# Optimization experiments

Hardware: AMD Instinct MI355X
Metric: run time of the kernel (lower is better)

The kernel has to match this reference:

```python
import jax, jax.numpy as jnp
import numpy as np

B, S, D, H = 2, 2048, 1024, 16
HD = D // H


def setup_inputs() -> dict:
    key = jax.random.key(0)
    ks = jax.random.split(key, 12)
    s = 0.02
    inp = {
        "query": jax.random.normal(ks[0], (B, S, D), dtype=jnp.float32),
        "Wq": jax.random.normal(ks[1], (D, D), dtype=jnp.float32) * s,
        "bq": jnp.zeros((D,), jnp.float32),
        "Wk": jax.random.normal(ks[2], (D, D), dtype=jnp.float32) * s,
        "bk": jnp.zeros((D,), jnp.float32),
        "Wv": jax.random.normal(ks[3], (D, D), dtype=jnp.float32) * s,
        "bv": jnp.zeros((D,), jnp.float32),
        "Wo": jax.random.normal(ks[4], (D, D), dtype=jnp.float32) * s,
        "bo": jnp.zeros((D,), jnp.float32),
        "Wm1": jax.random.normal(ks[5], (D // 4, D), dtype=jnp.float32) * s,
        "bm1": jnp.zeros((D // 4,), jnp.float32),
        "Wm2": jax.random.normal(ks[6], (D, D // 4), dtype=jnp.float32) * s,
        "bm2": jnp.zeros((D,), jnp.float32),
        "dopamine": jnp.ones((1,), jnp.float32),
        "serotonin": jnp.ones((1,), jnp.float32),
        "norepinephrine": jnp.ones((1,), jnp.float32),
        "acetylcholine": jnp.ones((1,), jnp.float32),
        "attention_scale": jnp.ones((1,), jnp.float32),
        "attention_bias": jnp.zeros((1,), jnp.float32),
    }
    return inp


def reference(query, Wq, bq, Wk, bk, Wv, bv, Wo, bo, Wm1, bm1, Wm2, bm2,
              dopamine, serotonin, norepinephrine, acetylcholine,
              attention_scale, attention_bias):
    b, s, d = query.shape
    scale = HD ** -0.5
    split = lambda t: t.reshape(b, s, H, HD).transpose(0, 2, 1, 3)  # [b,h,s,hd]
    q = split(query @ Wq.T + bq)
    k = split(query @ Wk.T + bk)
    v = split(query @ Wv.T + bv)
    scores = jnp.einsum('bhqd,bhkd->bhqk', q, k) * scale
    w = jax.nn.softmax(scores, axis=-1)  # dropout=0 (eval)
    attn = jnp.einsum('bhqk,bhkd->bhqd', w, v)
    # neuromodulation MLP on flattened query, then combined scalar gate
    mod = jax.nn.relu(query @ Wm1.T + bm1) @ Wm2.T + bm2  # [b,s,d]
    gate = (dopamine + serotonin + norepinephrine + acetylcholine) / 4.0  # [1]
    neuro = split(mod * gate)  # [b,h,s,hd]
    attn = (attn * attention_scale + attention_bias) * (1.0 + neuro)
    out = attn.transpose(0, 2, 1, 3).reshape(b, s, d) @ Wo.T + bo
    return out
```

## Files before the change

### kernel.cpp

```cpp
#include <hip/hip_runtime.h>
#include <stdint.h>
#include <math.h>


typedef __attribute__((ext_vector_type(8))) short short8;
typedef __attribute__((ext_vector_type(4))) float floatx4;

#define MFMA16(a, b, c) __builtin_amdgcn_mfma_f32_16x16x32_bf16(a, b, c, 0, 0, 0)

__device__ __forceinline__ unsigned short f2bf(float f) {
    union { float f; uint32_t u; } v; v.f = f;
    uint32_t r = v.u + 0x7fffu + ((v.u >> 16) & 1u);
    return (unsigned short)(r >> 16);
}
__device__ __forceinline__ float bf2f(unsigned short s) {
    union { uint32_t u; float f; } v; v.u = ((uint32_t)s) << 16;
    return v.f;
}

typedef const __attribute__((address_space(1))) void gvoid_t;
typedef __attribute__((address_space(3))) void lvoid_t;
__device__ __forceinline__ void gld16(const void* g, void* l) {
    __builtin_amdgcn_global_load_lds((gvoid_t*)g, (lvoid_t*)l, 16, 0, 0);
}

template<int BN, bool OUTBF>
__device__ __forceinline__ void gemm_core(const unsigned short* __restrict__ A,
                                          const unsigned short* __restrict__ W,
                                          const float* __restrict__ bias,
                                          void* __restrict__ C,
                                          int N, int K, int bm, int bn, bool relu)
{
    constexpr int MT = (BN == 128) ? 4 : 2;
    constexpr int SU = (BN == 128) ? 4 : 3;
    __shared__ __align__(16) unsigned short As[128][32];
    __shared__ __align__(16) unsigned short Ws[BN][32];

    const int tid  = threadIdx.x;
    const int w    = tid >> 6, lane = tid & 63;
    const int ln   = lane & 15, quad = lane >> 4;
    const int wm   = (BN == 128) ? (w >> 1) * 64 : w * 32;
    const int wn   = (BN == 128) ? (w & 1) * 64 : 0;

    floatx4 acc[MT][4] = {};

    for (int k0 = 0; k0 < K; k0 += 32) {
        __syncthreads();
        #pragma unroll
        for (int i = 0; i < SU; i++) {
            const int t = w * SU + i;
            if (t < 8) {
                const int r0  = t * 16;
                const int row = r0 + (lane >> 2);
                const int c   = (lane & 3) ^ ((row >> 1) & 3);
                gld16(&A[(size_t)(bm + row) * K + k0 + c * 8], &As[r0][0]);
            } else {
                const int r0  = (t - 8) * 16;
                const int row = r0 + (lane >> 2);
                const int c   = (lane & 3) ^ ((row >> 1) & 3);
                gld16(&W[(size_t)(bn + row) * K + k0 + c * 8], &Ws[r0][0]);
            }
        }
        __syncthreads();

        short8 af[MT], bf[4];
        #pragma unroll
        for (int mt = 0; mt < MT; mt++) {
            const int row = wm + mt * 16 + ln;
            af[mt] = *(const short8*)&As[row][(quad ^ ((row >> 1) & 3)) * 8];
        }
        #pragma unroll
        for (int nt = 0; nt < 4; nt++) {
            const int row = wn + nt * 16 + ln;
            bf[nt] = *(const short8*)&Ws[row][(quad ^ ((row >> 1) & 3)) * 8];
        }
        #pragma unroll
        for (int mt = 0; mt < MT; mt++)
            #pragma unroll
            for (int nt = 0; nt < 4; nt++)
                acc[mt][nt] = MFMA16(af[mt], bf[nt], acc[mt][nt]);
    }

    float bv[4];
    #pragma unroll
    for (int nt = 0; nt < 4; nt++) bv[nt] = bias[bn + wn + nt * 16 + ln];

    #pragma unroll
    for (int mt = 0; mt < MT; mt++) {
        #pragma unroll
        for (int nt = 0; nt < 4; nt++) {
            #pragma unroll
            for (int r = 0; r < 4; r++) {
                float v = acc[mt][nt][r] + bv[nt];
                if (relu) v = fmaxf(v, 0.f);
                const size_t row = (size_t)bm + wm + mt * 16 + quad * 4 + r;
                const size_t col = (size_t)bn + wn + nt * 16 + ln;
                if (OUTBF) ((unsigned short*)C)[row * N + col] = f2bf(v);
                else       ((float*)C)[row * N + col] = v;
            }
        }
    }
}

__global__ __launch_bounds__(256) void qkv_mlp1_gemm(
    const unsigned short* __restrict__ A,
    const unsigned short* __restrict__ Wq, const unsigned short* __restrict__ Wk,
    const unsigned short* __restrict__ Wv, const unsigned short* __restrict__ Wm1,
    const float* __restrict__ bq, const float* __restrict__ bk,
    const float* __restrict__ bv, const float* __restrict__ bm1,
    unsigned short* __restrict__ Qo, unsigned short* __restrict__ Ko,
    unsigned short* __restrict__ Vo, unsigned short* __restrict__ Ho)
{
    const int bx = blockIdx.x, bm = blockIdx.y * 128;
    const unsigned short* W; const float* bias; unsigned short* C;
    int N, bn; bool relu = false;
    if (bx < 8)       { W = Wq;  bias = bq;  C = Qo; N = 1024; bn = bx * 128; }
    else if (bx < 16) { W = Wk;  bias = bk;  C = Ko; N = 1024; bn = (bx - 8) * 128; }
    else if (bx < 24) { W = Wv;  bias = bv;  C = Vo; N = 1024; bn = (bx - 16) * 128; }
    else              { W = Wm1; bias = bm1; C = Ho; N = 256;  bn = (bx - 24) * 128; relu = true; }
    gemm_core<128, true>(A, W, bias, C, N, 1024, bm, bn, relu);
}

template<bool OUTBF>
__global__ __launch_bounds__(256) void gemm_bn64(const unsigned short* __restrict__ A,
                                                 const unsigned short* __restrict__ W,
                                                 const float* __restrict__ bias,
                                                 void* __restrict__ C, int N, int K)
{
    gemm_core<64, OUTBF>(A, W, bias, C, N, K, blockIdx.y * 128, blockIdx.x * 64, false);
}

__global__ __launch_bounds__(256) void attn_mfma(const unsigned short* __restrict__ Qg,
                                                 const unsigned short* __restrict__ Kg,
                                                 const unsigned short* __restrict__ Vtg,
                                                 const unsigned short* __restrict__ Modg,
                                                 unsigned short* __restrict__ Yg,
                                                 const float* __restrict__ dop,
                                                 const float* __restrict__ ser,
                                                 const float* __restrict__ nor,
                                                 const float* __restrict__ ach,
                                                 const float* __restrict__ asc,
                                                 const float* __restrict__ abi)
{
    __shared__ __align__(16) unsigned short Ks[128][64];
    __shared__ __align__(16) unsigned short Vs[64][128];
    __shared__ __align__(16) unsigned short Ps[4][16][128];

    const int tid = threadIdx.x;
    const int w   = tid >> 6, lane = tid & 63;
    const int ln  = lane & 15, quad = lane >> 4;
    const int qt  = blockIdx.x, h = blockIdx.y, b = blockIdx.z;

    const size_t qrow = (size_t)b * 2048 + qt * 64 + w * 16 + ln;
    const unsigned short* qp = Qg + qrow * 1024 + h * 64;
    const short8 qf0 = *(const short8*)&qp[quad * 8];
    const short8 qf1 = *(const short8*)&qp[32 + quad * 8];

    const size_t kbase = (size_t)b * 2048 * 1024 + h * 64;
    const size_t vbase = (size_t)(b * 16 + h) * 64 * 2048;

    floatx4 o[4] = {};
    float lsum[4] = {0.f, 0.f, 0.f, 0.f};

    for (int kc = 0; kc < 16; kc++) {
        __syncthreads();
        #pragma unroll
        for (int i = 0; i < 8; i++) {
            const int t = w * 8 + i;
            if (t < 16) {
                const int row = t * 8 + (lane >> 3);
                const int c   = (lane & 7) ^ (row & 7);
                gld16(&Kg[kbase + (size_t)(kc * 128 + row) * 1024 + c * 8], &Ks[t * 8][0]);
            } else {
                const int tv  = t - 16;
                const int row = tv * 4 + (lane >> 4);
                const int c   = (lane & 15) ^ (row & 7);
                gld16(&Vtg[vbase + (size_t)row * 2048 + kc * 128 + c * 8], &Vs[tv * 4][0]);
            }
        }
        __syncthreads();

        floatx4 sc[8];
        #pragma unroll
        for (int nt = 0; nt < 8; nt++) {
            const int row = nt * 16 + ln;
            const short8 kf0 = *(const short8*)&Ks[row][((0 + quad) ^ (ln & 7)) * 8];
            const short8 kf1 = *(const short8*)&Ks[row][((4 + quad) ^ (ln & 7)) * 8];
            floatx4 z = {};
            z = MFMA16(qf0, kf0, z);
            z = MFMA16(qf1, kf1, z);
            sc[nt] = z;
        }

        #pragma unroll
        for (int nt = 0; nt < 8; nt++) {
            #pragma unroll
            for (int r = 0; r < 4; r++) {
                const float p = __expf(sc[nt][r] * 0.125f);
                lsum[r] += p;
                const int prow = quad * 4 + r;
                const int col  = nt * 16 + ln;
                const int slot = (col >> 3) ^ (prow & 7);
                Ps[w][prow][slot * 8 + (ln & 7)] = f2bf(p);
            }
        }

        short8 pf[4];
        #pragma unroll
        for (int ks = 0; ks < 4; ks++)
            pf[ks] = *(const short8*)&Ps[w][ln][((4 * ks + quad) ^ (ln & 7)) * 8];

        #pragma unroll
        for (int ntv = 0; ntv < 4; ntv++) {
            const int row = ntv * 16 + ln;
            #pragma unroll
            for (int ks = 0; ks < 4; ks++) {
                const short8 vf = *(const short8*)&Vs[row][((4 * ks + quad) ^ (ln & 7)) * 8];
                o[ntv] = MFMA16(pf[ks], vf, o[ntv]);
            }
        }
    }

    #pragma unroll
    for (int r = 0; r < 4; r++) {
        float s = lsum[r];
        s += __shfl_xor(s, 1); s += __shfl_xor(s, 2);
        s += __shfl_xor(s, 4); s += __shfl_xor(s, 8);
        lsum[r] = 1.f / s;
    }

    const float gate = 0.25f * (dop[0] + ser[0] + nor[0] + ach[0]);
    const float scb = asc[0], bib = abi[0];
    const size_t orow0 = (size_t)b * 2048 + qt * 64 + w * 16;
    #pragma unroll
    for (int ntv = 0; ntv < 4; ntv++) {
        #pragma unroll
        for (int r = 0; r < 4; r++) {
            const size_t row = orow0 + quad * 4 + r;
            const size_t col = (size_t)h * 64 + ntv * 16 + ln;
            const float x  = o[ntv][r] * lsum[r];
            const float mo = bf2f(Modg[row * 1024 + col]);
            const float y  = (x * scb + bib) * (1.f + mo * gate);
            Yg[row * 1024 + col] = f2bf(y);
        }
    }
}

typedef __attribute__((ext_vector_type(8))) unsigned short ushort8;
__global__ __launch_bounds__(256) void transpose_v(const unsigned short* __restrict__ Vb,
                                                   unsigned short* __restrict__ Vt)
{
    __shared__ __align__(16) unsigned short T[64][72];
    const int tid = threadIdx.x;
    const int s0 = blockIdx.x * 64, h = blockIdx.y, b = blockIdx.z;
    const int g = tid & 7;
    #pragma unroll
    for (int p = 0; p < 2; p++) {
        const int row = p * 32 + (tid >> 3);
        const ushort8 v = *(const ushort8*)&Vb[(size_t)(b * 2048 + s0 + row) * 1024 + h * 64 + g * 8];
        *(ushort8*)&T[row][g * 8] = v;
    }
    __syncthreads();
    #pragma unroll
    for (int p = 0; p < 2; p++) {
        const int hd = p * 32 + (tid >> 3);
        ushort8 ov;
        #pragma unroll
        for (int j = 0; j < 8; j++) ov[j] = T[g * 8 + j][hd];
        *(ushort8*)&Vt[((size_t)(b * 16 + h) * 64 + hd) * 2048 + s0 + g * 8] = ov;
    }
}

__global__ __launch_bounds__(256) void fused_cast(
    const float* __restrict__ q,   const float* __restrict__ wq,
    const float* __restrict__ wk,  const float* __restrict__ wv,
    const float* __restrict__ wo,  const float* __restrict__ wm1,
    const float* __restrict__ wm2,
    unsigned short* __restrict__ dq,  unsigned short* __restrict__ dwq,
    unsigned short* __restrict__ dwk, unsigned short* __restrict__ dwv,
    unsigned short* __restrict__ dwo, unsigned short* __restrict__ dwm1,
    unsigned short* __restrict__ dwm2)
{
    const size_t u = (size_t)blockIdx.x * 256 + threadIdx.x;
    const float* src; unsigned short* dst; size_t off;
    if      (u <  524288) { src = q;   dst = dq;   off = u; }
    else if (u <  655360) { src = wq;  dst = dwq;  off = u - 524288; }
    else if (u <  786432) { src = wk;  dst = dwk;  off = u - 655360; }
    else if (u <  917504) { src = wv;  dst = dwv;  off = u - 786432; }
    else if (u < 1048576) { src = wo;  dst = dwo;  off = u - 917504; }
    else if (u < 1081344) { src = wm1; dst = dwm1; off = u - 1048576; }
    else                  { src = wm2; dst = dwm2; off = u - 1081344; }
    const float4* p = (const float4*)src + off * 2;
    const float4 a = p[0], c = p[1];
    ushort8 o;
    o[0] = f2bf(a.x); o[1] = f2bf(a.y); o[2] = f2bf(a.z); o[3] = f2bf(a.w);
    o[4] = f2bf(c.x); o[5] = f2bf(c.y); o[6] = f2bf(c.z); o[7] = f2bf(c.w);
    *(ushort8*)&dst[off * 8] = o;
}

extern "C" void kernel_launch(void* const* d_in, const int* in_sizes, int n_in,
                              void* d_out, int out_size, void* d_ws, size_t ws_size,
                              hipStream_t stream)
{
    const float* query = (const float*)d_in[0];
    const float* Wq  = (const float*)d_in[1];
    const float* bq  = (const float*)d_in[2];
    const float* Wk  = (const float*)d_in[3];
    const float* bk  = (const float*)d_in[4];
    const float* Wv  = (const float*)d_in[5];
    const float* bv  = (const float*)d_in[6];
    const float* Wo  = (const float*)d_in[7];
    const float* bo  = (const float*)d_in[8];
    const float* Wm1 = (const float*)d_in[9];
    const float* bm1 = (const float*)d_in[10];
    const float* Wm2 = (const float*)d_in[11];
    const float* bm2 = (const float*)d_in[12];
    const float* dop = (const float*)d_in[13];
    const float* ser = (const float*)d_in[14];
    const float* nor = (const float*)d_in[15];
    const float* ach = (const float*)d_in[16];
    const float* asc = (const float*)d_in[17];
    const float* abi = (const float*)d_in[18];

    char* ws = (char*)d_ws;
    const size_t MB = 1024 * 1024;
    unsigned short* Qry  = (unsigned short*)(ws);
    unsigned short* Wqb  = (unsigned short*)(ws + 8 * MB);
    unsigned short* Wkb  = (unsigned short*)(ws + 10 * MB);
    unsigned short* Wvb  = (unsigned short*)(ws + 12 * MB);
    unsigned short* Wob  = (unsigned short*)(ws + 14 * MB);
    unsigned short* Wm1b = (unsigned short*)(ws + 16 * MB);
    unsigned short* Wm2b = (unsigned short*)(ws + 16 * MB + 512 * 1024);
    unsigned short* Qb   = (unsigned short*)(ws + 17 * MB);
    unsigned short* Kb   = (unsigned short*)(ws + 25 * MB);
    unsigned short* Vb   = (unsigned short*)(ws + 33 * MB);
    unsigned short* Vt   = (unsigned short*)(ws + 41 * MB);
    unsigned short* Yb   = (unsigned short*)(ws + 49 * MB);
    unsigned short* Hm   = (unsigned short*)(ws + 57 * MB);
    unsigned short* Modb = Vb;

    fused_cast<<<4352, 256, 0, stream>>>(query, Wq, Wk, Wv, Wo, Wm1, Wm2,
                                         Qry, Wqb, Wkb, Wvb, Wob, Wm1b, Wm2b);

    qkv_mlp1_gemm<<<dim3(26, 32), 256, 0, stream>>>(
        Qry, Wqb, Wkb, Wvb, Wm1b, bq, bk, bv, bm1, Qb, Kb, Vb, Hm);

    transpose_v<<<dim3(32, 16, 2), 256, 0, stream>>>(Vb, Vt);

    gemm_bn64<true><<<dim3(16, 32), 256, 0, stream>>>(Hm, Wm2b, bm2, (void*)Modb, 1024, 256);

    attn_mfma<<<dim3(32, 16, 2), 256, 0, stream>>>(Qb, Kb, Vt, Modb, Yb,
                                                   dop, ser, nor, ach, asc, abi);

    gemm_bn64<false><<<dim3(16, 32), 256, 0, stream>>>(Yb, Wob, bo, d_out, 1024, 1024);
}
```

Measured before the change: 271.7 us.

## Double attention query tile per block and compute transposed scores to halve K/V reloads

The attention kernel now handles 128 query rows per block (32 per wave, two 16-row groups), so each K/V tile staged in LDS is reused by twice as many queries and the grid is halved. Scores are computed as K·Q^T so each lane holds four consecutive keys, which are packed into 8-byte LDS stores for P, and the key chunk is processed in two 64-wide halves. The softmax scale 0.125 is folded into the Q projection epilogue, and the row-sum reduction becomes two cross-quad shuffles. This trades more registers and a smaller grid (512 blocks) for fewer global loads and cheaper P writes.

```diff
diff --git a/kernel.cpp b/kernel.cpp
--- a/kernel.cpp
+++ b/kernel.cpp
@@ -4,6 +4,7 @@
 
 
 typedef __attribute__((ext_vector_type(8))) short short8;
+typedef __attribute__((ext_vector_type(8))) unsigned short ushort8;
 typedef __attribute__((ext_vector_type(4))) float floatx4;
 
 #define MFMA16(a, b, c) __builtin_amdgcn_mfma_f32_16x16x32_bf16(a, b, c, 0, 0, 0)
@@ -29,7 +30,8 @@
                                           const unsigned short* __restrict__ W,
                                           const float* __restrict__ bias,
                                           void* __restrict__ C,
-                                          int N, int K, int bm, int bn, bool relu)
+                                          int N, int K, int bm, int bn,
+                                          bool relu, float osc)
 {
     constexpr int MT = (BN == 128) ? 4 : 2;
     constexpr int SU = (BN == 128) ? 4 : 3;
@@ -91,7 +93,7 @@
         for (int nt = 0; nt < 4; nt++) {
             #pragma unroll
             for (int r = 0; r < 4; r++) {
-                float v = acc[mt][nt][r] + bv[nt];
+                float v = (acc[mt][nt][r] + bv[nt]) * osc;
                 if (relu) v = fmaxf(v, 0.f);
                 const size_t row = (size_t)bm + wm + mt * 16 + quad * 4 + r;
                 const size_t col = (size_t)bn + wn + nt * 16 + ln;
@@ -113,12 +115,12 @@
 {
     const int bx = blockIdx.x, bm = blockIdx.y * 128;
     const unsigned short* W; const float* bias; unsigned short* C;
-    int N, bn; bool relu = false;
-    if (bx < 8)       { W = Wq;  bias = bq;  C = Qo; N = 1024; bn = bx * 128; }
+    int N, bn; bool relu = false; float osc = 1.f;
+    if (bx < 8)       { W = Wq;  bias = bq;  C = Qo; N = 1024; bn = bx * 128; osc = 0.125f; }
     else if (bx < 16) { W = Wk;  bias = bk;  C = Ko; N = 1024; bn = (bx - 8) * 128; }
     else if (bx < 24) { W = Wv;  bias = bv;  C = Vo; N = 1024; bn = (bx - 16) * 128; }
     else              { W = Wm1; bias = bm1; C = Ho; N = 256;  bn = (bx - 24) * 128; relu = true; }
-    gemm_core<128, true>(A, W, bias, C, N, 1024, bm, bn, relu);
+    gemm_core<128, true>(A, W, bias, C, N, 1024, bm, bn, relu, osc);
 }
 
 template<bool OUTBF>
@@ -127,7 +129,8 @@
                                                  const float* __restrict__ bias,
                                                  void* __restrict__ C, int N, int K)
 {
-    gemm_core<64, OUTBF>(A, W, bias, C, N, K, blockIdx.y * 128, blockIdx.x * 64, false);
+    gemm_core<64, OUTBF>(A, W, bias, C, N, K, blockIdx.y * 128, blockIdx.x * 64,
+                         false, 1.f);
 }
 
 __global__ __launch_bounds__(256) void attn_mfma(const unsigned short* __restrict__ Qg,
@@ -144,23 +147,27 @@
 {
     __shared__ __align__(16) unsigned short Ks[128][64];
     __shared__ __align__(16) unsigned short Vs[64][128];
-    __shared__ __align__(16) unsigned short Ps[4][16][128];
+    __shared__ __align__(16) unsigned short Ps[4][2][16][64];
 
     const int tid = threadIdx.x;
     const int w   = tid >> 6, lane = tid & 63;
     const int ln  = lane & 15, quad = lane >> 4;
     const int qt  = blockIdx.x, h = blockIdx.y, b = blockIdx.z;
 
-    const size_t qrow = (size_t)b * 2048 + qt * 64 + w * 16 + ln;
-    const unsigned short* qp = Qg + qrow * 1024 + h * 64;
-    const short8 qf0 = *(const short8*)&qp[quad * 8];
-    const short8 qf1 = *(const short8*)&qp[32 + quad * 8];
+    const size_t qrowbase = (size_t)b * 2048 + qt * 128 + w * 32;
+    short8 qf[2][2];
+    #pragma unroll
+    for (int q2 = 0; q2 < 2; q2++) {
+        const unsigned short* qp = Qg + (qrowbase + q2 * 16 + ln) * 1024 + h * 64;
+        qf[q2][0] = *(const short8*)&qp[quad * 8];
+        qf[q2][1] = *(const short8*)&qp[32 + quad * 8];
+    }
 
     const size_t kbase = (size_t)b * 2048 * 1024 + h * 64;
     const size_t vbase = (size_t)(b * 16 + h) * 64 * 2048;
 
-    floatx4 o[4] = {};
-    float lsum[4] = {0.f, 0.f, 0.f, 0.f};
+    floatx4 o[2][4] = {};
+    float lsum[2] = {0.f, 0.f};
 
     for (int kc = 0; kc < 16; kc++) {
         __syncthreads();
@@ -168,85 +175,98 @@
         for (int i = 0; i < 8; i++) {
             const int t = w * 8 + i;
             if (t < 16) {
-                const int row = t * 8 + (lane >> 3);
-                const int c   = (lane & 7) ^ (row & 7);
-                gld16(&Kg[kbase + (size_t)(kc * 128 + row) * 1024 + c * 8], &Ks[t * 8][0]);
+                const int R = t * 8 + (lane >> 3);
+                const int c = (lane & 7) ^ (R & 7);
+                gld16(&Kg[kbase + (size_t)(kc * 128 + R) * 1024 + c * 8], &Ks[t * 8][0]);
             } else {
-                const int tv  = t - 16;
-                const int row = tv * 4 + (lane >> 4);
-                const int c   = (lane & 15) ^ (row & 7);
-                gld16(&Vtg[vbase + (size_t)row * 2048 + kc * 128 + c * 8], &Vs[tv * 4][0]);
+                const int tv = t - 16;
+                const int R  = tv * 4 + (lane >> 4);
+                const int c  = (lane & 15) ^ (R & 15);
+                gld16(&Vtg[vbase + (size_t)R * 2048 + kc * 128 + c * 8], &Vs[tv * 4][0]);
             }
         }
         __syncthreads();
 
-        floatx4 sc[8];
-        #pragma unroll
-        for (int nt = 0; nt < 8; nt++) {
-            const int row = nt * 16 + ln;
-            const short8 kf0 = *(const short8*)&Ks[row][((0 + quad) ^ (ln & 7)) * 8];
-            const short8 kf1 = *(const short8*)&Ks[row][((4 + quad) ^ (ln & 7)) * 8];
-            floatx4 z = {};
-            z = MFMA16(qf0, kf0, z);
-            z = MFMA16(qf1, kf1, z);
-            sc[nt] = z;
-        }
-
-        #pragma unroll
-        for (int nt = 0; nt < 8; nt++) {
-            #pragma unroll
-            for (int r = 0; r < 4; r++) {
-                const float p = __expf(sc[nt][r] * 0.125f);
-                lsum[r] += p;
-                const int prow = quad * 4 + r;
-                const int col  = nt * 16 + ln;
-                const int slot = (col >> 3) ^ (prow & 7);
-                Ps[w][prow][slot * 8 + (ln & 7)] = f2bf(p);
-            }
-        }
-
-        short8 pf[4];
-        #pragma unroll
-        for (int ks = 0; ks < 4; ks++)
-            pf[ks] = *(const short8*)&Ps[w][ln][((4 * ks + quad) ^ (ln & 7)) * 8];
-
-        #pragma unroll
-        for (int ntv = 0; ntv < 4; ntv++) {
-            const int row = ntv * 16 + ln;
-            #pragma unroll
-            for (int ks = 0; ks < 4; ks++) {
-                const short8 vf = *(const short8*)&Vs[row][((4 * ks + quad) ^ (ln & 7)) * 8];
-                o[ntv] = MFMA16(pf[ks], vf, o[ntv]);
-            }
-        }
-    }
-
-    #pragma unroll
-    for (int r = 0; r < 4; r++) {
-        float s = lsum[r];
-        s += __shfl_xor(s, 1); s += __shfl_xor(s, 2);
-        s += __shfl_xor(s, 4); s += __shfl_xor(s, 8);
-        lsum[r] = 1.f / s;
+        #pragma unroll
+        for (int half = 0; half < 2; half++) {
+            #pragma unroll
+            for (int q2 = 0; q2 < 2; q2++) {
+                floatx4 sc[4];
+                #pragma unroll
+                for (int mt = 0; mt < 4; mt++) {
+                    const int row = half * 64 + mt * 16 + ln;
+                    const short8 kf0 = *(const short8*)&Ks[row][((0 + quad) ^ (ln & 7)) * 8];
+                    const short8 kf1 = *(const short8*)&Ks[row][((4 + quad) ^ (ln & 7)) * 8];
+                    floatx4 z = {};
+                    z = MFMA16(kf0, qf[q2][0], z);
+                    z = MFMA16(kf1, qf[q2][1], z);
+                    sc[mt] = z;
+                }
+                #pragma unroll
+                for (int mt = 0; mt < 4; mt++) {
+                    const float p0 = __expf(sc[mt][0]);
+                    const float p1 = __expf(sc[mt][1]);
+                    const float p2 = __expf(sc[mt][2]);
+                    const float p3 = __expf(sc[mt][3]);
+                    lsum[q2] += (p0 + p1) + (p2 + p3);
+                    uint2 pk;
+                    pk.x = (uint32_t)f2bf(p0) | ((uint32_t)f2bf(p1) << 16);
+                    pk.y = (uint32_t)f2bf(p2) | ((uint32_t)f2bf(p3) << 16);
+                    const int c2 = (mt * 2 + (quad >> 1)) ^ (ln & 7);
+                    *(uint2*)((char*)&Ps[w][q2][ln][0] + c2 * 16 + (quad & 1) * 8) = pk;
+                }
+            }
+
+            short8 pf[2][2];
+            #pragma unroll
+            for (int q2 = 0; q2 < 2; q2++)
+                #pragma unroll
+                for (int ks = 0; ks < 2; ks++) {
+                    const int c2 = (ks * 4 + quad) ^ (ln & 7);
+                    pf[q2][ks] = *(const short8*)((char*)&Ps[w][q2][ln][0] + c2 * 16);
+                }
+            #pragma unroll
+            for (int ntv = 0; ntv < 4; ntv++) {
+                const int vrow = ntv * 16 + ln;
+                #pragma unroll
+                for (int ks = 0; ks < 2; ks++) {
+                    const int c2 = (half * 8 + ks * 4 + quad) ^ (ln & 15);
+                    const short8 vf = *(const short8*)&Vs[vrow][c2 * 8];
+                    o[0][ntv] = MFMA16(pf[0][ks], vf, o[0][ntv]);
+                    o[1][ntv] = MFMA16(pf[1][ks], vf, o[1][ntv]);
+                }
+            }
+        }
+    }
+
+    #pragma unroll
+    for (int q2 = 0; q2 < 2; q2++) {
+        float s = lsum[q2];
+        s += __shfl_xor(s, 16);
+        s += __shfl_xor(s, 32);
+        lsum[q2] = s;
     }
 
     const float gate = 0.25f * (dop[0] + ser[0] + nor[0] + ach[0]);
     const float scb = asc[0], bib = abi[0];
-    const size_t orow0 = (size_t)b * 2048 + qt * 64 + w * 16;
-    #pragma unroll
-    for (int ntv = 0; ntv < 4; ntv++) {
+    #pragma unroll
+    for (int q2 = 0; q2 < 2; q2++) {
         #pragma unroll
         for (int r = 0; r < 4; r++) {
-            const size_t row = orow0 + quad * 4 + r;
-            const size_t col = (size_t)h * 64 + ntv * 16 + ln;
-            const float x  = o[ntv][r] * lsum[r];
-            const float mo = bf2f(Modg[row * 1024 + col]);
-            const float y  = (x * scb + bib) * (1.f + mo * gate);
-            Yg[row * 1024 + col] = f2bf(y);
-        }
-    }
-}
-
-typedef __attribute__((ext_vector_type(8))) unsigned short ushort8;
+            const float inv = 1.f / __shfl(lsum[q2], quad * 4 + r);
+            const size_t row = qrowbase + q2 * 16 + quad * 4 + r;
+            #pragma unroll
+            for (int ntv = 0; ntv < 4; ntv++) {
+                const size_t col = (size_t)h * 64 + ntv * 16 + ln;
+                const float x  = o[q2][ntv][r] * inv;
+                const float mo = bf2f(Modg[row * 1024 + col]);
+                const float y  = (x * scb + bib) * (1.f + mo * gate);
+                Yg[row * 1024 + col] = f2bf(y);
+            }
+        }
+    }
+}
+
 __global__ __launch_bounds__(256) void transpose_v(const unsigned short* __restrict__ Vb,
                                                    unsigned short* __restrict__ Vt)
 {
@@ -349,7 +369,7 @@
 
     gemm_bn64<true><<<dim3(16, 32), 256, 0, stream>>>(Hm, Wm2b, bm2, (void*)Modb, 1024, 256);
 
-    attn_mfma<<<dim3(32, 16, 2), 256, 0, stream>>>(Qb, Kb, Vt, Modb, Yb,
+    attn_mfma<<<dim3(16, 16, 2), 256, 0, stream>>>(Qb, Kb, Vt, Modb, Yb,
                                                    dop, ser, nor, ach, asc, abi);
 
     gemm_bn64<false><<<dim3(16, 32), 256, 0, stream>>>(Yb, Wob, bo, d_out, 1024, 1024);
```

New measurement: 255.5 us. 5.9% less time.
